# Performance work log

Hardware: AMD Instinct MI355X
Metric: run time of the kernel (lower is better)

Reference implementation:

```python
import jax, jax.numpy as jnp
import numpy as np

VOCAB, EMB, HID = 32000, 512, 1024
B, T = 16, 128


def setup_inputs() -> dict:
    key = jax.random.key(0)
    ks = jax.random.split(key, 12)
    bound = 1.0 / np.sqrt(HID)
    u = lambda k, shape: jax.random.uniform(k, shape, jnp.float32, -bound, bound)
    return {
        "sentence": jax.random.randint(ks[0], (B, T), 0, VOCAB),
        "emb": jax.random.normal(ks[1], (VOCAB, EMB), jnp.float32),
        "W_i": u(ks[2], (EMB + HID, HID)), "b_i": u(ks[3], (HID,)),
        "W_f": u(ks[4], (EMB + HID, HID)), "b_f": u(ks[5], (HID,)),
        "W_o": u(ks[6], (EMB + HID, HID)), "b_o": u(ks[7], (HID,)),
        "W_c": u(ks[8], (EMB + HID, HID)), "b_c": u(ks[9], (HID,)),
        "W_hq": u(ks[10], (HID, VOCAB)), "b_q": u(ks[11], (VOCAB,)),
    }


def reference(sentence, emb, W_i, b_i, W_f, b_f, W_o, b_o, W_c, b_c, W_hq, b_q):
    # [B,T,E] -> [T,B,E]
    x = jnp.swapaxes(emb[sentence], 0, 1)
    # Fuse the 4 gate matmuls into one concatenated-weight matmul (same math).
    W = jnp.concatenate([W_i, W_f, W_o, W_c], axis=1)  # [E+H, 4H]
    b = jnp.concatenate([b_i, b_f, b_o, b_c])          # [4H]
    h0 = jnp.zeros((x.shape[1], HID), x.dtype)

    def step(carry, xt):
        h, c = carry
        z = jnp.concatenate([xt, h], axis=1) @ W + b   # [B,4H]
        i, f, o, g = jnp.split(z, 4, axis=1)
        i, f, o = jax.nn.sigmoid(i), jax.nn.sigmoid(f), jax.nn.sigmoid(o)
        c = f * c + i * jnp.tanh(g)
        h = o * jnp.tanh(c)
        return (h, c), h

    _, hs = jax.lax.scan(step, (h0, h0), x)            # [T,B,H]
    out = jnp.einsum('tbh,hv->tbv', hs, W_hq) + b_q    # [T,B,V]
    return jnp.transpose(out, (1, 2, 0))               # [B,V,T] as in torch permute(1,2,0)
```

## Files before the change

### kernel.cpp

```cpp
#include <hip/hip_runtime.h>
#include <math.h>

typedef float f32x4 __attribute__((ext_vector_type(4)));
typedef short bf16x8 __attribute__((ext_vector_type(8)));
typedef unsigned short u16;
typedef unsigned int u32;
typedef unsigned long long u64;

__device__ __forceinline__ float bf2f(u16 v) {
    union { unsigned u; float f; } x; x.u = ((unsigned)v) << 16; return x.f;
}
__device__ __forceinline__ u16 f2bf(float f) {
    union { float f; unsigned u; } x; x.f = f;
    unsigned r = x.u + 0x7fff + ((x.u >> 16) & 1);
    return (u16)(r >> 16);
}

__device__ __forceinline__ void gload_lds16(const u16* g, u16* l) {
    __builtin_amdgcn_global_load_lds(
        (const __attribute__((address_space(1))) void*)g,
        (__attribute__((address_space(3))) void*)l, 16, 0, 0);
}

__global__ void gather_embed(const int* __restrict__ sent, const float* __restrict__ emb,
                             u16* __restrict__ xb) {
    int row = blockIdx.x;
    int t = row >> 4, b = row & 15;
    int idx = sent[b * 128 + t];
    float4 v = ((const float4*)(emb + (size_t)idx * 512))[threadIdx.x];
    ushort4 s = { f2bf(v.x), f2bf(v.y), f2bf(v.z), f2bf(v.w) };
    ((ushort4*)(xb + (size_t)row * 512))[threadIdx.x] = s;
}

__global__ void build_b4(const float* __restrict__ bi, const float* __restrict__ bf_,
                         const float* __restrict__ bo, const float* __restrict__ bc,
                         float* __restrict__ b4) {
    int i = blockIdx.x * 256 + threadIdx.x;
    const float* p = (i < 1024) ? bi : (i < 2048) ? bf_ : (i < 3072) ? bo : bc;
    b4[i] = p[i & 1023];
}

__global__ void transpose_cvt(const float* __restrict__ in, int ldin,
                              u16* __restrict__ out, int ldout) {
    __shared__ float tile[32][33];
    int rt = blockIdx.y * 32, ct = blockIdx.x * 32;
    int tid = threadIdx.x;
    int r = tid >> 3, cq = (tid & 7) * 4;
    float4 v = *(const float4*)(in + (size_t)(rt + r) * ldin + ct + cq);
    tile[r][cq] = v.x; tile[r][cq + 1] = v.y; tile[r][cq + 2] = v.z; tile[r][cq + 3] = v.w;
    __syncthreads();
    int c = tid >> 3, rq = (tid & 7) * 4;
    ushort4 s = { f2bf(tile[rq][c]), f2bf(tile[rq + 1][c]),
                  f2bf(tile[rq + 2][c]), f2bf(tile[rq + 3][c]) };
    *(ushort4*)(out + (size_t)(ct + c) * ldout + rt + rq) = s;
}

template <int MODE>
__global__ __launch_bounds__(256) void gemm_bt(
    const u16* __restrict__ A, const u16* __restrict__ Bt,
    const float* __restrict__ bias, float* __restrict__ C, int K) {
    const int tid = threadIdx.x;
    const int l = tid & 63, w = tid >> 6;
    const int wr = w >> 1, wc = w & 1;
    const int m0 = blockIdx.x * 128, n0 = blockIdx.y * 128;
    __shared__ __align__(16) u16 As[128 * 64];
    __shared__ __align__(16) u16 Bs[128 * 64];

    f32x4 acc[4][4];
    f32x4 zz = { 0.f, 0.f, 0.f, 0.f };
#pragma unroll
    for (int i = 0; i < 4; i++)
#pragma unroll
        for (int j = 0; j < 4; j++) acc[i][j] = zz;

    const int nkt = K >> 6;
    for (int kt = 0; kt < nkt; ++kt) {
        __syncthreads();
#pragma unroll
        for (int i = 0; i < 4; i++) {
            int cbase = i * 256 + w * 64;
            int c = cbase + l, row = c >> 3, kc = c & 7;
            int arow = (MODE == 1) ? (row * 16 + (int)blockIdx.x) : (m0 + row);
            gload_lds16(A + (size_t)arow * K + kt * 64 + kc * 8, As + (size_t)cbase * 8);
            gload_lds16(Bt + (size_t)(n0 + row) * K + kt * 64 + kc * 8, Bs + (size_t)cbase * 8);
        }
        __syncthreads();
#pragma unroll
        for (int kk = 0; kk < 2; kk++) {
            bf16x8 af[4], bfv[4];
#pragma unroll
            for (int mi = 0; mi < 4; mi++)
                af[mi] = *(const bf16x8*)(As + (wr * 64 + mi * 16 + (l & 15)) * 64 + kk * 32 + (l >> 4) * 8);
#pragma unroll
            for (int ni = 0; ni < 4; ni++)
                bfv[ni] = *(const bf16x8*)(Bs + (wc * 64 + ni * 16 + (l & 15)) * 64 + kk * 32 + (l >> 4) * 8);
#pragma unroll
            for (int mi = 0; mi < 4; mi++)
#pragma unroll
                for (int ni = 0; ni < 4; ni++)
                    acc[mi][ni] = __builtin_amdgcn_mfma_f32_16x16x32_bf16(af[mi], bfv[ni], acc[mi][ni], 0, 0, 0);
        }
    }
    const int lr = l >> 4, lc = l & 15;
#pragma unroll
    for (int ni = 0; ni < 4; ni++) {
        int col = n0 + wc * 64 + ni * 16 + lc;
        float bv = bias[col];
#pragma unroll
        for (int mi = 0; mi < 4; mi++) {
            if (MODE == 0) {
#pragma unroll
                for (int r = 0; r < 4; r++) {
                    int row = m0 + wr * 64 + mi * 16 + lr * 4 + r;
                    C[(size_t)row * 4096 + col] = acc[mi][ni][r] + bv;
                }
            } else {
                int t0 = wr * 64 + mi * 16 + lr * 4;
                float4 st = { acc[mi][ni][0] + bv, acc[mi][ni][1] + bv,
                              acc[mi][ni][2] + bv, acc[mi][ni][3] + bv };
                *(float4*)(C + (size_t)blockIdx.x * 4096000 + (size_t)col * 128 + t0) = st;
            }
        }
    }
}

#define FLAG_STRIDE 16
__global__ __launch_bounds__(256, 1) void lstm_rec(
    u16* __restrict__ hs,
    const float* __restrict__ xz,
    const float* __restrict__ Wi, const float* __restrict__ Wf,
    const float* __restrict__ Wo, const float* __restrict__ Wc,
    u32* __restrict__ flags) {
    __shared__ __align__(16) u16 hstage[16384];
    __shared__ float zlds[4][16][17];
    __shared__ u32 lds_cnt;
    const int j = blockIdx.x;
    const int tid = threadIdx.x;
    const int w = tid >> 6, l = tid & 63;
    const int row = l & 15, hi = l >> 4;
    const float* Wg = (w == 0) ? Wi : (w == 1) ? Wf : (w == 2) ? Wo : Wc;

    if (tid == 0) {
        lds_cnt = 0;
        __hip_atomic_fetch_add(&flags[(size_t)(128 * 64 + j) * FLAG_STRIDE], 0u,
                               __ATOMIC_ACQ_REL, __HIP_MEMORY_SCOPE_AGENT);
    }

    bf16x8 wf[32];
    {
#pragma unroll
        for (int kk = 0; kk < 32; ++kk)
#pragma unroll
            for (int e = 0; e < 8; ++e)
                wf[kk][e] = f2bf(Wg[(size_t)(512 + kk * 32 + hi * 8 + e) * 1024 + j * 16 + row]);
    }
    __syncthreads();

    const int b = tid >> 4, hc = tid & 15;
    float cst = 0.f;
    const float* xr0 = xz + (size_t)b * 4096 + j * 16 + hc;
    float cz0 = xr0[0], cz1 = xr0[1024], cz2 = xr0[2048], cz3 = xr0[3072];

    for (int t = 0; t < 128; ++t) {
        if (t > 0) {
            if (w == 0) {
                int spins = 0;
                while (true) {
                    u32 f = __hip_atomic_load(&flags[(size_t)((t - 1) * 64 + l) * FLAG_STRIDE],
                                              __ATOMIC_RELAXED, __HIP_MEMORY_SCOPE_SYSTEM);
                    if (__ballot(f != 0) == ~0ull) break;
                    __builtin_amdgcn_s_sleep(1);
                    if (++spins > (1 << 20)) break;
                }
            }
            __syncthreads();
            {
                const u16* hbase = hs + (size_t)(t - 1) * 16 * 1024;
#pragma unroll
                for (int q = 0; q < 8; ++q) {
                    int S = (w * 8 + q) * 64 + l;
                    int sr = S >> 7, ss = S & 127;
                    int c = (ss & ~7) | ((ss ^ sr) & 7);
                    gload_lds16(hbase + sr * 1024 + c * 8, hstage + (size_t)(w * 8 + q) * 512);
                }
            }
        }
        float nz0 = 0.f, nz1 = 0.f, nz2 = 0.f, nz3 = 0.f;
        if (t < 127) {
            const float* xr = xz + (size_t)((t + 1) * 16 + b) * 4096 + j * 16 + hc;
            nz0 = xr[0]; nz1 = xr[1024]; nz2 = xr[2048]; nz3 = xr[3072];
        }
        if (t > 0) {
            __syncthreads();
            f32x4 zv = { 0.f, 0.f, 0.f, 0.f };
            f32x4 ac0 = zv, ac1 = zv, ac2 = zv, ac3 = zv;
#pragma unroll
            for (int kk = 0; kk < 32; kk += 4) {
#pragma unroll
                for (int u = 0; u < 4; ++u) {
                    int c = (kk + u) * 4 + hi;
                    int s = (c & ~7) | ((c ^ row) & 7);
                    bf16x8 a = *(const bf16x8*)(hstage + row * 1024 + s * 8);
                    f32x4& ac = (u == 0) ? ac0 : (u == 1) ? ac1 : (u == 2) ? ac2 : ac3;
                    ac = __builtin_amdgcn_mfma_f32_16x16x32_bf16(a, wf[kk + u], ac, 0, 0, 0);
                }
            }
            f32x4 acc = (ac0 + ac1) + (ac2 + ac3);
#pragma unroll
            for (int r = 0; r < 4; ++r)
                zlds[w][hi * 4 + r][row] = acc[r];
        }
        __syncthreads();
        {
            float zi = cz0, zf = cz1, zo = cz2, zc = cz3;
            if (t > 0) {
                zi += zlds[0][b][hc]; zf += zlds[1][b][hc];
                zo += zlds[2][b][hc]; zc += zlds[3][b][hc];
            }
            float ig = 1.f / (1.f + __expf(-zi));
            float fg = 1.f / (1.f + __expf(-zf));
            float og = 1.f / (1.f + __expf(-zo));
            float gg = tanhf(zc);
            cst = fg * cst + ig * gg;
            float h = og * tanhf(cst);
            float hn = __shfl_xor(h, 1);
            if (!(l & 1)) {
                unsigned pk = (unsigned)f2bf(h) | ((unsigned)f2bf(hn) << 16);
                u32* dst = (u32*)hs + (((size_t)(t * 16 + b) * 1024 + j * 16 + hc) >> 1);
                __hip_atomic_store(dst, pk, __ATOMIC_RELAXED, __HIP_MEMORY_SCOPE_SYSTEM);
            }
        }
        cz0 = nz0; cz1 = nz1; cz2 = nz2; cz3 = nz3;
        asm volatile("s_waitcnt vmcnt(0)" ::: "memory");
        if (l == 0) {
            u32 old = atomicAdd(&lds_cnt, 1u);
            if (old == (u32)(4 * t + 3))
                __hip_atomic_store(&flags[(size_t)(t * 64 + j) * FLAG_STRIDE], 1u,
                                   __ATOMIC_RELAXED, __HIP_MEMORY_SCOPE_SYSTEM);
        }
    }
}

extern "C" void kernel_launch(void* const* d_in, const int* in_sizes, int n_in,
                              void* d_out, int out_size, void* d_ws, size_t ws_size,
                              hipStream_t stream) {
    const int*   sent = (const int*)d_in[0];
    const float* emb  = (const float*)d_in[1];
    const float* W_i  = (const float*)d_in[2];
    const float* b_i  = (const float*)d_in[3];
    const float* W_f  = (const float*)d_in[4];
    const float* b_f  = (const float*)d_in[5];
    const float* W_o  = (const float*)d_in[6];
    const float* b_o  = (const float*)d_in[7];
    const float* W_c  = (const float*)d_in[8];
    const float* b_c  = (const float*)d_in[9];
    const float* W_hq = (const float*)d_in[10];
    const float* b_q  = (const float*)d_in[11];
    float* out = (float*)d_out;

    char* ws = (char*)d_ws;
    size_t off = 0;
    auto alloc = [&](size_t bytes) { void* p = ws + off; off += (bytes + 255) & ~255ull; return p; };
    size_t flag_bytes = (size_t)(128 * 64 + 64) * 16 * 4;
    u32*   flags = (u32*)alloc(flag_bytes);
    float* b4   = (float*)alloc((size_t)4096 * 4);
    u16*   xb   = (u16*)alloc((size_t)2048 * 512 * 2);
    u16*   wxt  = (u16*)alloc((size_t)4096 * 512 * 2);
    u16*   hs   = (u16*)alloc((size_t)2048 * 1024 * 2);
    float* xz   = (float*)alloc((size_t)2048 * 4096 * 4);
    u16*   whqt = (u16*)alloc((size_t)32000 * 1024 * 2);

    hipMemsetAsync(flags, 0, flag_bytes, stream);
    gather_embed<<<2048, 128, 0, stream>>>(sent, emb, xb);
    build_b4<<<16, 256, 0, stream>>>(b_i, b_f, b_o, b_c, b4);
    transpose_cvt<<<dim3(32, 16), 256, 0, stream>>>(W_i, 1024, wxt + (size_t)0 * 1024 * 512, 512);
    transpose_cvt<<<dim3(32, 16), 256, 0, stream>>>(W_f, 1024, wxt + (size_t)1 * 1024 * 512, 512);
    transpose_cvt<<<dim3(32, 16), 256, 0, stream>>>(W_o, 1024, wxt + (size_t)2 * 1024 * 512, 512);
    transpose_cvt<<<dim3(32, 16), 256, 0, stream>>>(W_c, 1024, wxt + (size_t)3 * 1024 * 512, 512);
    transpose_cvt<<<dim3(1000, 32), 256, 0, stream>>>(W_hq, 32000, whqt, 1024);
    gemm_bt<0><<<dim3(16, 32), 256, 0, stream>>>(xb, wxt, b4, xz, 512);
    lstm_rec<<<64, 256, 0, stream>>>(hs, xz, W_i, W_f, W_o, W_c, flags);
    gemm_bt<1><<<dim3(16, 250), 256, 0, stream>>>(hs, whqt, b_q, out, 1024);
}
```

Before: 729.2 us.

## Overlap output projection with LSTM recurrence and merge prep kernels

Merges the embedding gather, bias build and all weight transposes into one prep launch. The recurrent LSTM and the vocabulary projection GEMM now run in one persistent launch. Projection blocks spin on per-timestep-chunk epoch flags and start computing 8-timestep slices while the recurrence continues. This hides the large output GEMM behind the serial recurrence and cuts launch count. The risks are that projection blocks may occupy CUs and memory bandwidth that the latency-critical recurrent blocks need (setprio is used to counter this), and that spin-waiting can deadlock if the 64 recurrent blocks are not all resident.

```diff
diff --git a/kernel.cpp b/kernel.cpp
--- a/kernel.cpp
+++ b/kernel.cpp
@@ -7,9 +7,12 @@
 typedef unsigned int u32;
 typedef unsigned long long u64;
 
-__device__ __forceinline__ float bf2f(u16 v) {
-    union { unsigned u; float f; } x; x.u = ((unsigned)v) << 16; return x.f;
-}
+#define FLAG_STRIDE 16
+#define FLAGS_TJ    8192
+#define ACQ_BASE    8192
+#define EPOCH_BASE  8448
+#define FLAG_WORDS  ((EPOCH_BASE + 64) * FLAG_STRIDE)
+
 __device__ __forceinline__ u16 f2bf(float f) {
     union { float f; unsigned u; } x; x.f = f;
     unsigned r = x.u + 0x7fff + ((x.u >> 16) & 1);
@@ -22,66 +25,76 @@
         (__attribute__((address_space(3))) void*)l, 16, 0, 0);
 }
 
-__global__ void gather_embed(const int* __restrict__ sent, const float* __restrict__ emb,
-                             u16* __restrict__ xb) {
-    int row = blockIdx.x;
-    int t = row >> 4, b = row & 15;
-    int idx = sent[b * 128 + t];
-    float4 v = ((const float4*)(emb + (size_t)idx * 512))[threadIdx.x];
-    ushort4 s = { f2bf(v.x), f2bf(v.y), f2bf(v.z), f2bf(v.w) };
-    ((ushort4*)(xb + (size_t)row * 512))[threadIdx.x] = s;
-}
-
-__global__ void build_b4(const float* __restrict__ bi, const float* __restrict__ bf_,
-                         const float* __restrict__ bo, const float* __restrict__ bc,
-                         float* __restrict__ b4) {
-    int i = blockIdx.x * 256 + threadIdx.x;
-    const float* p = (i < 1024) ? bi : (i < 2048) ? bf_ : (i < 3072) ? bo : bc;
-    b4[i] = p[i & 1023];
-}
-
-__global__ void transpose_cvt(const float* __restrict__ in, int ldin,
-                              u16* __restrict__ out, int ldout) {
+__global__ __launch_bounds__(256) void prep(
+    const int* __restrict__ sent, const float* __restrict__ emb, u16* __restrict__ xb,
+    const float* __restrict__ bi, const float* __restrict__ bf_,
+    const float* __restrict__ bo, const float* __restrict__ bc, float* __restrict__ b4,
+    const float* __restrict__ Wi, const float* __restrict__ Wf,
+    const float* __restrict__ Wo, const float* __restrict__ Wc, u16* __restrict__ wxt,
+    const float* __restrict__ Whq, u16* __restrict__ whqt) {
     __shared__ float tile[32][33];
-    int rt = blockIdx.y * 32, ct = blockIdx.x * 32;
-    int tid = threadIdx.x;
-    int r = tid >> 3, cq = (tid & 7) * 4;
-    float4 v = *(const float4*)(in + (size_t)(rt + r) * ldin + ct + cq);
-    tile[r][cq] = v.x; tile[r][cq + 1] = v.y; tile[r][cq + 2] = v.z; tile[r][cq + 3] = v.w;
-    __syncthreads();
-    int c = tid >> 3, rq = (tid & 7) * 4;
-    ushort4 s = { f2bf(tile[rq][c]), f2bf(tile[rq + 1][c]),
-                  f2bf(tile[rq + 2][c]), f2bf(tile[rq + 3][c]) };
-    *(ushort4*)(out + (size_t)(ct + c) * ldout + rt + rq) = s;
-}
-
-template <int MODE>
-__global__ __launch_bounds__(256) void gemm_bt(
+    const int bx = blockIdx.x, tid = threadIdx.x;
+    if (bx < 1024) {
+        int row = bx * 2 + (tid >> 7);
+        int t = row >> 4, b = row & 15;
+        int idx = sent[b * 128 + t];
+        float4 v = ((const float4*)(emb + (size_t)idx * 512))[tid & 127];
+        ushort4 s = { f2bf(v.x), f2bf(v.y), f2bf(v.z), f2bf(v.w) };
+        ((ushort4*)(xb + (size_t)row * 512))[tid & 127] = s;
+        return;
+    }
+    if (bx < 1040) {
+        int i = (bx - 1024) * 256 + tid;
+        const float* p = (i < 1024) ? bi : (i < 2048) ? bf_ : (i < 3072) ? bo : bc;
+        b4[i] = p[i & 1023];
+        return;
+    }
+    const float* in; u16* out; int ldin, ldout, rt, ct;
+    if (bx < 3088) {
+        int q = bx - 1040, g = q >> 9, r = q & 511;
+        in = (g == 0) ? Wi : (g == 1) ? Wf : (g == 2) ? Wo : Wc;
+        ldin = 1024; out = wxt + (size_t)g * 1024 * 512; ldout = 512;
+        rt = (r >> 5) * 32; ct = (r & 31) * 32;
+    } else {
+        int q = bx - 3088;
+        in = Whq; ldin = 32000; out = whqt; ldout = 1024;
+        rt = (q / 1000) * 32; ct = (q % 1000) * 32;
+    }
+    {
+        int r = tid >> 3, cq = (tid & 7) * 4;
+        float4 v = *(const float4*)(in + (size_t)(rt + r) * ldin + ct + cq);
+        tile[r][cq] = v.x; tile[r][cq + 1] = v.y; tile[r][cq + 2] = v.z; tile[r][cq + 3] = v.w;
+        __syncthreads();
+        int c = tid >> 3, rq = (tid & 7) * 4;
+        ushort4 s = { f2bf(tile[rq][c]), f2bf(tile[rq + 1][c]),
+                      f2bf(tile[rq + 2][c]), f2bf(tile[rq + 3][c]) };
+        *(ushort4*)(out + (size_t)(ct + c) * ldout + rt + rq) = s;
+    }
+}
+
+__global__ __launch_bounds__(256) void gemm_xz(
     const u16* __restrict__ A, const u16* __restrict__ Bt,
-    const float* __restrict__ bias, float* __restrict__ C, int K) {
+    const float* __restrict__ bias, float* __restrict__ C) {
     const int tid = threadIdx.x;
     const int l = tid & 63, w = tid >> 6;
     const int wr = w >> 1, wc = w & 1;
     const int m0 = blockIdx.x * 128, n0 = blockIdx.y * 128;
+    const int K = 512;
     __shared__ __align__(16) u16 As[128 * 64];
     __shared__ __align__(16) u16 Bs[128 * 64];
-
     f32x4 acc[4][4];
     f32x4 zz = { 0.f, 0.f, 0.f, 0.f };
 #pragma unroll
     for (int i = 0; i < 4; i++)
 #pragma unroll
         for (int j = 0; j < 4; j++) acc[i][j] = zz;
-
-    const int nkt = K >> 6;
-    for (int kt = 0; kt < nkt; ++kt) {
+    for (int kt = 0; kt < (K >> 6); ++kt) {
         __syncthreads();
 #pragma unroll
         for (int i = 0; i < 4; i++) {
             int cbase = i * 256 + w * 64;
             int c = cbase + l, row = c >> 3, kc = c & 7;
-            int arow = (MODE == 1) ? (row * 16 + (int)blockIdx.x) : (m0 + row);
-            gload_lds16(A + (size_t)arow * K + kt * 64 + kc * 8, As + (size_t)cbase * 8);
+            gload_lds16(A + (size_t)(m0 + row) * K + kt * 64 + kc * 8, As + (size_t)cbase * 8);
             gload_lds16(Bt + (size_t)(n0 + row) * K + kt * 64 + kc * 8, Bs + (size_t)cbase * 8);
         }
         __syncthreads();
@@ -107,136 +120,222 @@
         int col = n0 + wc * 64 + ni * 16 + lc;
         float bv = bias[col];
 #pragma unroll
-        for (int mi = 0; mi < 4; mi++) {
-            if (MODE == 0) {
-#pragma unroll
-                for (int r = 0; r < 4; r++) {
-                    int row = m0 + wr * 64 + mi * 16 + lr * 4 + r;
-                    C[(size_t)row * 4096 + col] = acc[mi][ni][r] + bv;
-                }
-            } else {
-                int t0 = wr * 64 + mi * 16 + lr * 4;
-                float4 st = { acc[mi][ni][0] + bv, acc[mi][ni][1] + bv,
-                              acc[mi][ni][2] + bv, acc[mi][ni][3] + bv };
-                *(float4*)(C + (size_t)blockIdx.x * 4096000 + (size_t)col * 128 + t0) = st;
-            }
-        }
-    }
-}
-
-#define FLAG_STRIDE 16
-__global__ __launch_bounds__(256, 1) void lstm_rec(
+        for (int mi = 0; mi < 4; mi++)
+#pragma unroll
+            for (int r = 0; r < 4; r++) {
+                int row = m0 + wr * 64 + mi * 16 + lr * 4 + r;
+                C[(size_t)row * 4096 + col] = acc[mi][ni][r] + bv;
+            }
+    }
+}
+
+__global__ __launch_bounds__(256, 1) void lstm_proj(
     u16* __restrict__ hs,
     const float* __restrict__ xz,
     const float* __restrict__ Wi, const float* __restrict__ Wf,
     const float* __restrict__ Wo, const float* __restrict__ Wc,
-    u32* __restrict__ flags) {
-    __shared__ __align__(16) u16 hstage[16384];
-    __shared__ float zlds[4][16][17];
-    __shared__ u32 lds_cnt;
-    const int j = blockIdx.x;
+    u32* __restrict__ flags,
+    const u16* __restrict__ whqt,
+    const float* __restrict__ bq, float* __restrict__ out) {
+    __shared__ __align__(16) char smem[37632];
+    const int bx = blockIdx.x;
     const int tid = threadIdx.x;
     const int w = tid >> 6, l = tid & 63;
-    const int row = l & 15, hi = l >> 4;
-    const float* Wg = (w == 0) ? Wi : (w == 1) ? Wf : (w == 2) ? Wo : Wc;
-
-    if (tid == 0) {
-        lds_cnt = 0;
-        __hip_atomic_fetch_add(&flags[(size_t)(128 * 64 + j) * FLAG_STRIDE], 0u,
+
+    if (tid == 0)
+        __hip_atomic_fetch_add(&flags[(size_t)(ACQ_BASE + (bx & 255)) * FLAG_STRIDE], 0u,
                                __ATOMIC_ACQ_REL, __HIP_MEMORY_SCOPE_AGENT);
-    }
-
-    bf16x8 wf[32];
-    {
+
+    if (bx < 64) {
+        u16* hstage = (u16*)smem;
+        float (*zlds)[16][17] = (float (*)[16][17])(void*)(smem + 32768);
+        u32* lds_cnt = (u32*)(smem + 37120);
+        const int j = bx;
+        const int row = l & 15, hi = l >> 4;
+        const float* Wg = (w == 0) ? Wi : (w == 1) ? Wf : (w == 2) ? Wo : Wc;
+        if (tid == 0) *lds_cnt = 0;
+        __builtin_amdgcn_s_setprio(1);
+
+        bf16x8 wf[32];
 #pragma unroll
         for (int kk = 0; kk < 32; ++kk)
 #pragma unroll
             for (int e = 0; e < 8; ++e)
                 wf[kk][e] = f2bf(Wg[(size_t)(512 + kk * 32 + hi * 8 + e) * 1024 + j * 16 + row]);
-    }
-    __syncthreads();
-
-    const int b = tid >> 4, hc = tid & 15;
-    float cst = 0.f;
-    const float* xr0 = xz + (size_t)b * 4096 + j * 16 + hc;
-    float cz0 = xr0[0], cz1 = xr0[1024], cz2 = xr0[2048], cz3 = xr0[3072];
-
-    for (int t = 0; t < 128; ++t) {
-        if (t > 0) {
-            if (w == 0) {
-                int spins = 0;
-                while (true) {
-                    u32 f = __hip_atomic_load(&flags[(size_t)((t - 1) * 64 + l) * FLAG_STRIDE],
-                                              __ATOMIC_RELAXED, __HIP_MEMORY_SCOPE_SYSTEM);
-                    if (__ballot(f != 0) == ~0ull) break;
-                    __builtin_amdgcn_s_sleep(1);
-                    if (++spins > (1 << 20)) break;
-                }
+        __syncthreads();
+
+        const int b = tid >> 4, hc = tid & 15;
+        float cst = 0.f;
+        const float* xr0 = xz + (size_t)b * 4096 + j * 16 + hc;
+        float cz0 = xr0[0], cz1 = xr0[1024], cz2 = xr0[2048], cz3 = xr0[3072];
+
+        for (int t = 0; t < 128; ++t) {
+            if (t > 0) {
+                if (w == 0) {
+                    __builtin_amdgcn_s_setprio(0);
+                    int spins = 0;
+                    while (true) {
+                        u32 f = __hip_atomic_load(&flags[(size_t)((t - 1) * 64 + l) * FLAG_STRIDE],
+                                                  __ATOMIC_RELAXED, __HIP_MEMORY_SCOPE_SYSTEM);
+                        if (__ballot(f != 0) == ~0ull) break;
+                        __builtin_amdgcn_s_sleep(1);
+                        if (++spins > (1 << 20)) break;
+                    }
+                    __builtin_amdgcn_s_setprio(1);
+                    if (l == 0)
+                        __hip_atomic_store(&flags[(size_t)(EPOCH_BASE + j) * FLAG_STRIDE], (u32)t,
+                                           __ATOMIC_RELAXED, __HIP_MEMORY_SCOPE_SYSTEM);
+                }
+                __syncthreads();
+                {
+                    const u16* hbase = hs + (size_t)(t - 1) * 16 * 1024;
+#pragma unroll
+                    for (int q = 0; q < 8; ++q) {
+                        int S = (w * 8 + q) * 64 + l;
+                        int sr = S >> 7, ss = S & 127;
+                        int c = (ss & ~7) | ((ss ^ sr) & 7);
+                        gload_lds16(hbase + sr * 1024 + c * 8, hstage + (size_t)(w * 8 + q) * 512);
+                    }
+                }
+            }
+            float nz0 = 0.f, nz1 = 0.f, nz2 = 0.f, nz3 = 0.f;
+            if (t < 127) {
+                const float* xr = xz + (size_t)((t + 1) * 16 + b) * 4096 + j * 16 + hc;
+                nz0 = xr[0]; nz1 = xr[1024]; nz2 = xr[2048]; nz3 = xr[3072];
+            }
+            if (t > 0) {
+                __syncthreads();
+                f32x4 zv = { 0.f, 0.f, 0.f, 0.f };
+                f32x4 ac0 = zv, ac1 = zv, ac2 = zv, ac3 = zv;
+#pragma unroll
+                for (int kk = 0; kk < 32; kk += 4) {
+#pragma unroll
+                    for (int u = 0; u < 4; ++u) {
+                        int c = (kk + u) * 4 + hi;
+                        int s = (c & ~7) | ((c ^ row) & 7);
+                        bf16x8 a = *(const bf16x8*)(hstage + row * 1024 + s * 8);
+                        f32x4& ac = (u == 0) ? ac0 : (u == 1) ? ac1 : (u == 2) ? ac2 : ac3;
+                        ac = __builtin_amdgcn_mfma_f32_16x16x32_bf16(a, wf[kk + u], ac, 0, 0, 0);
+                    }
+                }
+                f32x4 acc = (ac0 + ac1) + (ac2 + ac3);
+#pragma unroll
+                for (int r = 0; r < 4; ++r)
+                    zlds[w][hi * 4 + r][row] = acc[r];
             }
             __syncthreads();
             {
-                const u16* hbase = hs + (size_t)(t - 1) * 16 * 1024;
-#pragma unroll
-                for (int q = 0; q < 8; ++q) {
-                    int S = (w * 8 + q) * 64 + l;
-                    int sr = S >> 7, ss = S & 127;
-                    int c = (ss & ~7) | ((ss ^ sr) & 7);
-                    gload_lds16(hbase + sr * 1024 + c * 8, hstage + (size_t)(w * 8 + q) * 512);
-                }
-            }
-        }
-        float nz0 = 0.f, nz1 = 0.f, nz2 = 0.f, nz3 = 0.f;
-        if (t < 127) {
-            const float* xr = xz + (size_t)((t + 1) * 16 + b) * 4096 + j * 16 + hc;
-            nz0 = xr[0]; nz1 = xr[1024]; nz2 = xr[2048]; nz3 = xr[3072];
-        }
-        if (t > 0) {
-            __syncthreads();
-            f32x4 zv = { 0.f, 0.f, 0.f, 0.f };
-            f32x4 ac0 = zv, ac1 = zv, ac2 = zv, ac3 = zv;
-#pragma unroll
-            for (int kk = 0; kk < 32; kk += 4) {
-#pragma unroll
-                for (int u = 0; u < 4; ++u) {
-                    int c = (kk + u) * 4 + hi;
-                    int s = (c & ~7) | ((c ^ row) & 7);
-                    bf16x8 a = *(const bf16x8*)(hstage + row * 1024 + s * 8);
-                    f32x4& ac = (u == 0) ? ac0 : (u == 1) ? ac1 : (u == 2) ? ac2 : ac3;
-                    ac = __builtin_amdgcn_mfma_f32_16x16x32_bf16(a, wf[kk + u], ac, 0, 0, 0);
-                }
-            }
-            f32x4 acc = (ac0 + ac1) + (ac2 + ac3);
-#pragma unroll
-            for (int r = 0; r < 4; ++r)
-                zlds[w][hi * 4 + r][row] = acc[r];
-        }
-        __syncthreads();
-        {
-            float zi = cz0, zf = cz1, zo = cz2, zc = cz3;
-            if (t > 0) {
-                zi += zlds[0][b][hc]; zf += zlds[1][b][hc];
-                zo += zlds[2][b][hc]; zc += zlds[3][b][hc];
-            }
-            float ig = 1.f / (1.f + __expf(-zi));
-            float fg = 1.f / (1.f + __expf(-zf));
-            float og = 1.f / (1.f + __expf(-zo));
-            float gg = tanhf(zc);
-            cst = fg * cst + ig * gg;
-            float h = og * tanhf(cst);
-            float hn = __shfl_xor(h, 1);
-            if (!(l & 1)) {
-                unsigned pk = (unsigned)f2bf(h) | ((unsigned)f2bf(hn) << 16);
-                u32* dst = (u32*)hs + (((size_t)(t * 16 + b) * 1024 + j * 16 + hc) >> 1);
-                __hip_atomic_store(dst, pk, __ATOMIC_RELAXED, __HIP_MEMORY_SCOPE_SYSTEM);
-            }
-        }
-        cz0 = nz0; cz1 = nz1; cz2 = nz2; cz3 = nz3;
-        asm volatile("s_waitcnt vmcnt(0)" ::: "memory");
-        if (l == 0) {
-            u32 old = atomicAdd(&lds_cnt, 1u);
-            if (old == (u32)(4 * t + 3))
-                __hip_atomic_store(&flags[(size_t)(t * 64 + j) * FLAG_STRIDE], 1u,
+                float zi = cz0, zf = cz1, zo = cz2, zc = cz3;
+                if (t > 0) {
+                    zi += zlds[0][b][hc]; zf += zlds[1][b][hc];
+                    zo += zlds[2][b][hc]; zc += zlds[3][b][hc];
+                }
+                float ig = 1.f / (1.f + __expf(-zi));
+                float fg = 1.f / (1.f + __expf(-zf));
+                float og = 1.f / (1.f + __expf(-zo));
+                float gg = tanhf(zc);
+                cst = fg * cst + ig * gg;
+                float h = og * tanhf(cst);
+                float hn = __shfl_xor(h, 1);
+                if (!(l & 1)) {
+                    unsigned pk = (unsigned)f2bf(h) | ((unsigned)f2bf(hn) << 16);
+                    u32* dst = (u32*)hs + (((size_t)(t * 16 + b) * 1024 + j * 16 + hc) >> 1);
+                    __hip_atomic_store(dst, pk, __ATOMIC_RELAXED, __HIP_MEMORY_SCOPE_SYSTEM);
+                }
+            }
+            cz0 = nz0; cz1 = nz1; cz2 = nz2; cz3 = nz3;
+            asm volatile("s_waitcnt vmcnt(0)" ::: "memory");
+            if (l == 0) {
+                u32 old = atomicAdd(lds_cnt, 1u);
+                if (old == (u32)(4 * t + 3))
+                    __hip_atomic_store(&flags[(size_t)(t * 64 + j) * FLAG_STRIDE], 1u,
+                                       __ATOMIC_RELAXED, __HIP_MEMORY_SCOPE_SYSTEM);
+            }
+        }
+        if (w == 0) {
+            int spins = 0;
+            while (true) {
+                u32 f = __hip_atomic_load(&flags[(size_t)(127 * 64 + l) * FLAG_STRIDE],
+                                          __ATOMIC_RELAXED, __HIP_MEMORY_SCOPE_SYSTEM);
+                if (__ballot(f != 0) == ~0ull) break;
+                __builtin_amdgcn_s_sleep(1);
+                if (++spins > (1 << 20)) break;
+            }
+            if (l == 0)
+                __hip_atomic_store(&flags[(size_t)(EPOCH_BASE + j) * FLAG_STRIDE], 128u,
                                    __ATOMIC_RELAXED, __HIP_MEMORY_SCOPE_SYSTEM);
+        }
+        return;
+    }
+
+    u16* As = (u16*)smem;
+    u16* Bs = (u16*)(smem + 16384);
+    const int pid = bx - 64;
+    const int mchunk = pid / 250;
+    const int n0 = (pid % 250) * 128;
+    const int wr = w >> 1, wc = w & 1;
+
+    if (w == 0) {
+        const u32 need = (u32)(8 * mchunk + 8);
+        int spins = 0;
+        while (true) {
+            u32 e = __hip_atomic_load(&flags[(size_t)(EPOCH_BASE + (pid & 63)) * FLAG_STRIDE],
+                                      __ATOMIC_RELAXED, __HIP_MEMORY_SCOPE_SYSTEM);
+            if (e >= need) break;
+            __builtin_amdgcn_s_sleep(32);
+            if (++spins > (1 << 17)) break;
+        }
+    }
+    __syncthreads();
+
+    f32x4 acc[4][4];
+    f32x4 zz = { 0.f, 0.f, 0.f, 0.f };
+#pragma unroll
+    for (int i = 0; i < 4; i++)
+#pragma unroll
+        for (int jj = 0; jj < 4; jj++) acc[i][jj] = zz;
+
+    const int K = 1024;
+    for (int kt = 0; kt < 16; ++kt) {
+        __syncthreads();
+#pragma unroll
+        for (int i = 0; i < 4; i++) {
+            int cbase = i * 256 + w * 64;
+            int c = cbase + l, row = c >> 3, kc = c & 7;
+            int arow = (8 * mchunk + (row & 7)) * 16 + (row >> 3);
+            gload_lds16(hs + (size_t)arow * K + kt * 64 + kc * 8, As + (size_t)cbase * 8);
+            gload_lds16(whqt + (size_t)(n0 + row) * K + kt * 64 + kc * 8, Bs + (size_t)cbase * 8);
+        }
+        __syncthreads();
+#pragma unroll
+        for (int kk = 0; kk < 2; kk++) {
+            bf16x8 af[4], bfv[4];
+#pragma unroll
+            for (int mi = 0; mi < 4; mi++)
+                af[mi] = *(const bf16x8*)(As + (wr * 64 + mi * 16 + (l & 15)) * 64 + kk * 32 + (l >> 4) * 8);
+#pragma unroll
+            for (int ni = 0; ni < 4; ni++)
+                bfv[ni] = *(const bf16x8*)(Bs + (wc * 64 + ni * 16 + (l & 15)) * 64 + kk * 32 + (l >> 4) * 8);
+#pragma unroll
+            for (int mi = 0; mi < 4; mi++)
+#pragma unroll
+                for (int ni = 0; ni < 4; ni++)
+                    acc[mi][ni] = __builtin_amdgcn_mfma_f32_16x16x32_bf16(af[mi], bfv[ni], acc[mi][ni], 0, 0, 0);
+        }
+    }
+    const int lr = l >> 4, lc = l & 15;
+#pragma unroll
+    for (int ni = 0; ni < 4; ni++) {
+        int col = n0 + wc * 64 + ni * 16 + lc;
+        float bv = bq[col];
+#pragma unroll
+        for (int mi = 0; mi < 4; mi++) {
+            int r0 = wr * 64 + mi * 16 + lr * 4;
+            int bb = r0 >> 3;
+            int t0 = 8 * mchunk + (r0 & 7);
+            float4 st = { acc[mi][ni][0] + bv, acc[mi][ni][1] + bv,
+                          acc[mi][ni][2] + bv, acc[mi][ni][3] + bv };
+            *(float4*)(out + (size_t)bb * 4096000 + (size_t)col * 128 + t0) = st;
         }
     }
 }
@@ -261,8 +360,7 @@
     char* ws = (char*)d_ws;
     size_t off = 0;
     auto alloc = [&](size_t bytes) { void* p = ws + off; off += (bytes + 255) & ~255ull; return p; };
-    size_t flag_bytes = (size_t)(128 * 64 + 64) * 16 * 4;
-    u32*   flags = (u32*)alloc(flag_bytes);
+    u32*   flags = (u32*)alloc((size_t)FLAG_WORDS * 4);
     float* b4   = (float*)alloc((size_t)4096 * 4);
     u16*   xb   = (u16*)alloc((size_t)2048 * 512 * 2);
     u16*   wxt  = (u16*)alloc((size_t)4096 * 512 * 2);
@@ -270,15 +368,10 @@
     float* xz   = (float*)alloc((size_t)2048 * 4096 * 4);
     u16*   whqt = (u16*)alloc((size_t)32000 * 1024 * 2);
 
-    hipMemsetAsync(flags, 0, flag_bytes, stream);
-    gather_embed<<<2048, 128, 0, stream>>>(sent, emb, xb);
-    build_b4<<<16, 256, 0, stream>>>(b_i, b_f, b_o, b_c, b4);
-    transpose_cvt<<<dim3(32, 16), 256, 0, stream>>>(W_i, 1024, wxt + (size_t)0 * 1024 * 512, 512);
-    transpose_cvt<<<dim3(32, 16), 256, 0, stream>>>(W_f, 1024, wxt + (size_t)1 * 1024 * 512, 512);
-    transpose_cvt<<<dim3(32, 16), 256, 0, stream>>>(W_o, 1024, wxt + (size_t)2 * 1024 * 512, 512);
-    transpose_cvt<<<dim3(32, 16), 256, 0, stream>>>(W_c, 1024, wxt + (size_t)3 * 1024 * 512, 512);
-    transpose_cvt<<<dim3(1000, 32), 256, 0, stream>>>(W_hq, 32000, whqt, 1024);
-    gemm_bt<0><<<dim3(16, 32), 256, 0, stream>>>(xb, wxt, b4, xz, 512);
-    lstm_rec<<<64, 256, 0, stream>>>(hs, xz, W_i, W_f, W_o, W_c, flags);
-    gemm_bt<1><<<dim3(16, 250), 256, 0, stream>>>(hs, whqt, b_q, out, 1024);
-}
+    hipMemsetAsync(flags, 0, (size_t)FLAG_WORDS * 4, stream);
+    prep<<<35088, 256, 0, stream>>>(sent, emb, xb, b_i, b_f, b_o, b_c, b4,
+                                    W_i, W_f, W_o, W_c, wxt, W_hq, whqt);
+    gemm_xz<<<dim3(16, 32), 256, 0, stream>>>(xb, wxt, b4, xz);
+    lstm_proj<<<64 + 16 * 250, 256, 0, stream>>>(hs, xz, W_i, W_f, W_o, W_c,
+                                                 flags, whqt, b_q, out);
+}
```

Result: slower. 773.0 us (+6.0%).
